# Performance work log

Measured on AMD Instinct MI355X. Metric: run time of the kernel, lower is better.

Reference implementation:

```python
import jax, jax.numpy as jnp
import numpy as np

BLOCK_CONFIGS = [[4, 64, 64], [64, 128, 128], [128, 256, 256], [256, 512]]
KNN_K = 16
PN, PL, PM = 5, 3, 3          # kernel polynomial degrees (N, L, M)
BASIS = PN * PL * PM          # 45 monomial basis functions
NUM_LAYERS = 4
N_POINTS = 32768


def get_reduction_schedule(n_input, n_target, num_layers):
    # geometric point-count reduction from n_input down to n_target
    r = (n_target / n_input) ** (1.0 / num_layers)
    return [max(n_target, int(round(n_input * r ** (i + 1)))) for i in range(num_layers)]


def knn_idx(qpos, spos, k):
    # squared distances via the |q|^2 + |s|^2 - 2 q.s identity (avoids (q,s,3) temp)
    d = jnp.sum(qpos * qpos, 1)[:, None] + jnp.sum(spos * spos, 1)[None, :] - 2.0 * (qpos @ spos.T)
    _, idx = jax.lax.top_k(-d, k)  # (q, k) nearest-neighbor indices
    return idx


def poly_basis(r):
    # monomial basis x^i y^j z^k, i<PN, j<PL, k<PM -> (q, k, BASIS)
    x, y, z = r[..., 0], r[..., 1], r[..., 2]
    px = x[..., None] ** jnp.arange(PN)
    py = y[..., None] ** jnp.arange(PL)
    pz = z[..., None] ** jnp.arange(PM)
    phi = px[..., :, None, None] * py[..., None, :, None] * pz[..., None, None, :]
    return phi.reshape(r.shape[:-1] + (BASIS,))


def dcconv(qpos, spos, sfeat, k, W, b, use_pca=True):
    # KNN gather -> normalized relative coords -> (PCA align) -> polynomial kernel conv
    idx = knn_idx(qpos, spos, k)
    r = spos[idx] - qpos[:, None, :]                         # (q, k, 3)
    scale = jnp.max(jnp.sqrt(jnp.sum(r * r, -1)), axis=-1, keepdims=True)
    r = r / (scale[..., None] + 1e-8)
    if use_pca:
        cov = jnp.einsum('qki,qkj->qij', r, r) / k           # (q, 3, 3)
        _, vecs = jnp.linalg.eigh(cov)
        vecs = jax.lax.stop_gradient(vecs)                   # PCA frame treated as constant
        r = jnp.einsum('qki,qij->qkj', r, vecs)
    phi = poly_basis(r)                                       # (q, k, B)
    nf = sfeat[idx]                                           # (q, k, Cin)
    t = jnp.einsum('qkb,qkc->qbc', phi, nf) / k               # neighbor reduce (mean)
    return jnp.einsum('qbc,bco->qo', t, W) + b


def _forward(position_matrix, channel_matrix, ws, bs, ps, head_w, head_b):
    sched = get_reduction_schedule(position_matrix.shape[0], 1, NUM_LAYERS)
    pos, feat = position_matrix, channel_matrix
    li = 0
    for bi, cfg in enumerate(BLOCK_CONFIGS):
        n_sel = sched[bi]
        qpos = pos[:n_sel]                                    # selector: first n_sel centers
        res = feat[:n_sel] @ ps[bi]                           # residual projection
        x, src_pos = feat, pos
        for _ in range(len(cfg) - 1):
            k = min(KNN_K, src_pos.shape[0])
            x = jax.nn.relu(dcconv(qpos, src_pos, x, k, ws[li], bs[li]))
            li += 1
            src_pos = qpos                                    # subsequent layers: self-conv on reduced set
        feat = jax.nn.relu(x + res)
        pos = qpos
    if feat.shape[0] > 1:
        feat = feat.mean(0, keepdims=True)
    return (feat @ head_w + head_b)[0]                        # (out_channels,) = (1,)


def setup_inputs():
    key = jax.random.key(0)
    ks = jax.random.split(key, 32)
    inp = {}
    inp['position_matrix'] = jax.random.normal(ks[0], (N_POINTS, 3), dtype=jnp.float32)
    inp['channel_matrix'] = jax.random.normal(ks[1], (N_POINTS, 4), dtype=jnp.float32)
    i, li = 2, 1
    for cfg in BLOCK_CONFIGS:
        for cin, cout in zip(cfg[:-1], cfg[1:]):
            inp[f'w{li}'] = jax.random.normal(ks[i], (BASIS, cin, cout), dtype=jnp.float32) * 0.05
            inp[f'b{li}'] = jnp.zeros((cout,), dtype=jnp.float32)
            i += 1
            li += 1
    for bi, cfg in enumerate(BLOCK_CONFIGS):
        inp[f'p{bi + 1}'] = jax.random.normal(ks[i], (cfg[0], cfg[-1]), dtype=jnp.float32) * 0.05
        i += 1
    inp['head_w'] = jax.random.normal(ks[i], (BLOCK_CONFIGS[-1][-1], 1), dtype=jnp.float32) * 0.05
    inp['head_b'] = jnp.zeros((1,), dtype=jnp.float32)
    return inp


def reference(position_matrix, channel_matrix, w1, b1, w2, b2, w3, b3, w4, b4, w5, b5, w6, b6, w7, b7,
              p1, p2, p3, p4, head_w, head_b):
    ws = [w1, w2, w3, w4, w5, w6, w7]
    bs = [b1, b2, b3, b4, b5, b6, b7]
    ps = [p1, p2, p3, p4]
    return _forward(position_matrix, channel_matrix, ws, bs, ps, head_w, head_b)
```

## Files before the change

kernel.cpp:

```cpp
#include <hip/hip_runtime.h>
#include <math.h>

#pragma clang fp contract(off)

__device__ __forceinline__ float f_sign(float a, float b) {
    return (b >= 0.0f) ? fabsf(a) : -fabsf(a);
}

__device__ float slapy2(float x, float y) {
    float xa = fabsf(x), ya = fabsf(y);
    float w = fmaxf(xa, ya), z = fminf(xa, ya);
    if (z == 0.0f) return w;
    float t = z / w;
    return w * sqrtf(1.0f + t * t);
}

__device__ void slartg(float f, float g, float &cs, float &sn, float &r) {
    if (g == 0.0f) { cs = 1.0f; sn = 0.0f; r = f; }
    else if (f == 0.0f) { cs = 0.0f; sn = f_sign(1.0f, g); r = fabsf(g); }
    else {
        float d = sqrtf(f * f + g * g);
        float p = 1.0f / d;
        cs = fabsf(f) * p;
        sn = g * f_sign(p, f);
        r = f_sign(d, f);
    }
}

__device__ void slaev2(float a, float b, float c,
                       float &rt1, float &rt2, float &cs1, float &sn1) {
    float sm = a + c, df = a - c, adf = fabsf(df), tb = b + b, ab = fabsf(tb);
    float acmx, acmn;
    if (fabsf(a) > fabsf(c)) { acmx = a; acmn = c; } else { acmx = c; acmn = a; }
    float rt;
    if (adf > ab) { float t = ab / adf; rt = adf * sqrtf(1.0f + t * t); }
    else if (adf < ab) { float t = adf / ab; rt = ab * sqrtf(1.0f + t * t); }
    else rt = ab * sqrtf(2.0f);
    int sgn1;
    if (sm < 0.0f) { rt1 = 0.5f * (sm - rt); sgn1 = -1; rt2 = (acmx / rt1) * acmn - (b / rt1) * b; }
    else if (sm > 0.0f) { rt1 = 0.5f * (sm + rt); sgn1 = 1; rt2 = (acmx / rt1) * acmn - (b / rt1) * b; }
    else { rt1 = 0.5f * rt; rt2 = -0.5f * rt; sgn1 = 1; }
    float cs; int sgn2;
    if (df >= 0.0f) { cs = df + rt; sgn2 = 1; } else { cs = df - rt; sgn2 = -1; }
    float acs = fabsf(cs);
    if (acs > ab) { float ct = -tb / cs; sn1 = 1.0f / sqrtf(1.0f + ct * ct); cs1 = ct * sn1; }
    else {
        if (ab == 0.0f) { cs1 = 1.0f; sn1 = 0.0f; }
        else { float tn = -cs / tb; cs1 = 1.0f / sqrtf(1.0f + tn * tn); sn1 = tn * cs1; }
    }
    if (sgn1 == sgn2) { float tn = cs1; cs1 = -sn1; sn1 = tn; }
}

__device__ void ssteqr3(float *d, float *e, float z[3][3]) {
    const int n = 3;
    const float eps = 5.9604644775390625e-08f;
    const float eps2 = eps * eps;
    const float safmin = 1.1754943508222875e-38f;
    for (int i = 0; i < 3; ++i)
        for (int j = 0; j < 3; ++j)
            z[i][j] = (i == j) ? 1.0f : 0.0f;
    const int nmaxit = n * 30;
    int jtot = 0;
    int l1 = 1;
    int l, m, lend;
    float p, g, r, c, s, f, b, rt1, rt2;
    float wc[2], wsn[2];

L10:
    if (l1 > n) goto L160;
    if (l1 > 1) e[l1 - 2] = 0.0f;
    if (l1 <= n - 1) {
        for (m = l1; m <= n - 1; ++m) {
            float tst = fabsf(e[m - 1]);
            if (tst == 0.0f) goto L30;
            if (tst <= (sqrtf(fabsf(d[m - 1])) * sqrtf(fabsf(d[m]))) * eps) {
                e[m - 1] = 0.0f;
                goto L30;
            }
        }
    }
    m = n;
L30:
    l = l1;
    lend = m;
    l1 = m + 1;
    if (lend == l) goto L10;
    {
        float anorm = 0.0f;
        for (int i = l; i <= lend; ++i) anorm = fmaxf(anorm, fabsf(d[i - 1]));
        for (int i = l; i <= lend - 1; ++i) anorm = fmaxf(anorm, fabsf(e[i - 1]));
        if (anorm == 0.0f) goto L10;
    }
    if (fabsf(d[lend - 1]) < fabsf(d[l - 1])) { int t = lend; lend = l; l = t; }

    if (lend > l) {
L40:
        if (l != lend) {
            bool found = false;
            for (m = l; m <= lend - 1; ++m) {
                float tst = e[m - 1] * e[m - 1];
                if (tst <= (eps2 * fabsf(d[m - 1])) * fabsf(d[m]) + safmin) { found = true; break; }
            }
            if (!found) m = lend;
        } else m = lend;
        if (m < lend) e[m - 1] = 0.0f;
        p = d[l - 1];
        if (m == l) goto L80;
        if (m == l + 1) {
            slaev2(d[l - 1], e[l - 1], d[l], rt1, rt2, c, s);
            for (int i = 0; i < n; ++i) {
                float tmp = z[i][l];
                z[i][l]     = c * tmp - s * z[i][l - 1];
                z[i][l - 1] = s * tmp + c * z[i][l - 1];
            }
            d[l - 1] = rt1; d[l] = rt2; e[l - 1] = 0.0f;
            l += 2;
            if (l <= lend) goto L40;
            goto L140;
        }
        if (jtot == nmaxit) goto L140;
        ++jtot;
        g = (d[l] - p) / (2.0f * e[l - 1]);
        r = slapy2(g, 1.0f);
        g = (d[m - 1] - p) + e[l - 1] / (g + f_sign(r, g));
        s = 1.0f; c = 1.0f; p = 0.0f;
        for (int i = m - 1; i >= l; --i) {
            f = s * e[i - 1];
            b = c * e[i - 1];
            slartg(g, f, c, s, r);
            if (i != m - 1) e[i] = r;
            g = d[i] - p;
            r = (d[i - 1] - g) * s + (2.0f * c) * b;
            p = s * r;
            d[i] = g + p;
            g = c * r - b;
            wc[i - 1] = c;
            wsn[i - 1] = -s;
        }
        for (int jj = m - 1; jj >= l; --jj) {
            float ct = wc[jj - 1], st = wsn[jj - 1];
            for (int i = 0; i < n; ++i) {
                float tmp = z[i][jj];
                z[i][jj]     = ct * tmp - st * z[i][jj - 1];
                z[i][jj - 1] = st * tmp + ct * z[i][jj - 1];
            }
        }
        d[l - 1] -= p;
        e[l - 1] = g;
        goto L40;
L80:
        d[l - 1] = p;
        ++l;
        if (l <= lend) goto L40;
        goto L140;
    } else {
L90:
        if (l != lend) {
            bool found = false;
            for (m = l; m >= lend + 1; --m) {
                float tst = e[m - 2] * e[m - 2];
                if (tst <= (eps2 * fabsf(d[m - 1])) * fabsf(d[m - 2]) + safmin) { found = true; break; }
            }
            if (!found) m = lend;
        } else m = lend;
        if (m > lend) e[m - 2] = 0.0f;
        p = d[l - 1];
        if (m == l) goto L130;
        if (m == l - 1) {
            slaev2(d[l - 2], e[l - 2], d[l - 1], rt1, rt2, c, s);
            for (int i = 0; i < n; ++i) {
                float tmp = z[i][l - 1];
                z[i][l - 1] = c * tmp - s * z[i][l - 2];
                z[i][l - 2] = s * tmp + c * z[i][l - 2];
            }
            d[l - 2] = rt1; d[l - 1] = rt2; e[l - 2] = 0.0f;
            l -= 2;
            if (l >= lend) goto L90;
            goto L140;
        }
        if (jtot == nmaxit) goto L140;
        ++jtot;
        g = (d[l - 2] - p) / (2.0f * e[l - 2]);
        r = slapy2(g, 1.0f);
        g = (d[m - 1] - p) + e[l - 2] / (g + f_sign(r, g));
        s = 1.0f; c = 1.0f; p = 0.0f;
        for (int i = m; i <= l - 1; ++i) {
            f = s * e[i - 1];
            b = c * e[i - 1];
            slartg(g, f, c, s, r);
            if (i != m) e[i - 2] = r;
            g = d[i - 1] - p;
            r = (d[i] - g) * s + (2.0f * c) * b;
            p = s * r;
            d[i - 1] = g + p;
            g = c * r - b;
            wc[i - 1] = c;
            wsn[i - 1] = s;
        }
        for (int jj = m; jj <= l - 1; ++jj) {
            float ct = wc[jj - 1], st = wsn[jj - 1];
            for (int i = 0; i < n; ++i) {
                float tmp = z[i][jj];
                z[i][jj]     = ct * tmp - st * z[i][jj - 1];
                z[i][jj - 1] = st * tmp + ct * z[i][jj - 1];
            }
        }
        d[l - 1] -= p;
        e[l - 2] = g;
        goto L90;
L130:
        d[l - 1] = p;
        --l;
        if (l >= lend) goto L90;
        goto L140;
    }
L140:
    if (jtot < nmaxit) goto L10;
L160:
    for (int ii = 2; ii <= n; ++ii) {
        int i = ii - 1, kk = i;
        float pp = d[i - 1];
        for (int j = ii; j <= n; ++j)
            if (d[j - 1] < pp) { kk = j; pp = d[j - 1]; }
        if (kk != i) {
            d[kk - 1] = d[i - 1];
            d[i - 1] = pp;
            for (int row = 0; row < n; ++row) {
                float t2 = z[row][i - 1];
                z[row][i - 1] = z[row][kk - 1];
                z[row][kk - 1] = t2;
            }
        }
    }
}

__device__ void ssyevd3(float a11, float a21, float a31,
                        float a22, float a32, float a33, float V[3][3]) {
    float tau1, v2, e1;
    float alpha = a21;
    float xnorm = fabsf(a31);
    if (xnorm == 0.0f) {
        tau1 = 0.0f; v2 = 0.0f; e1 = a21;
    } else {
        float beta = -f_sign(slapy2(alpha, xnorm), alpha);
        tau1 = (beta - alpha) / beta;
        float t = 1.0f / (alpha - beta);
        v2 = a31 * t;
        e1 = beta;
        float w1 = tau1 * a22;
        float w2 = tau1 * a32;
        float temp2 = a32 * v2;
        w1 = w1 + tau1 * temp2;
        float temp1 = tau1 * v2;
        w2 = w2 + temp1 * a33;
        float dot = w1;
        dot = dot + w2 * v2;
        float alpha2 = (-0.5f * tau1) * dot;
        w1 = w1 + alpha2;
        w2 = w2 + alpha2 * v2;
        a22 = (a22 - w1) - w1;
        a32 = (a32 - v2 * w1) - w2;
        a33 = (a33 - v2 * w2) - w2 * v2;
    }
    float d[3] = { a11, a22, a33 };
    float e[2] = { e1, a32 };
    float z[3][3];
    ssteqr3(d, e, z);
    for (int j = 0; j < 3; ++j) {
        float wj = z[1][j];
        wj = wj + z[2][j] * v2;
        float temp = (-tau1) * wj;
        V[0][j] = z[0][j];
        V[1][j] = z[1][j] + temp;
        V[2][j] = z[2][j] + v2 * temp;
    }
}

__device__ void geom_body(const float *__restrict__ posf, const int *__restrict__ ord,
                          int q, int k, float *__restrict__ rrot) {
    float qx = posf[3 * q], qy = posf[3 * q + 1], qz = posf[3 * q + 2];
    float rx[16], ry[16], rz[16], nrm[16];
    for (int j = 0; j < k; ++j) {
        int s = ord[j];
        rx[j] = posf[3 * s] - qx;
        ry[j] = posf[3 * s + 1] - qy;
        rz[j] = posf[3 * s + 2] - qz;
        float t = rx[j] * rx[j];
        t = t + ry[j] * ry[j];
        t = t + rz[j] * rz[j];
        nrm[j] = sqrtf(t);
    }
    float scale = nrm[0];
    for (int j = 1; j < k; ++j) scale = fmaxf(scale, nrm[j]);
    float sc = scale + 1e-8f;
    for (int j = 0; j < k; ++j) {
        rx[j] = rx[j] / sc;
        ry[j] = ry[j] / sc;
        rz[j] = rz[j] / sc;
    }
    float c00 = 0.f, c01 = 0.f, c02 = 0.f, c11 = 0.f, c12 = 0.f, c22 = 0.f;
    for (int j = 0; j < k; ++j) {
        c00 = c00 + rx[j] * rx[j];
        c01 = c01 + rx[j] * ry[j];
        c02 = c02 + rx[j] * rz[j];
        c11 = c11 + ry[j] * ry[j];
        c12 = c12 + ry[j] * rz[j];
        c22 = c22 + rz[j] * rz[j];
    }
    float fk = (float)k;
    c00 = c00 / fk; c01 = c01 / fk; c02 = c02 / fk;
    c11 = c11 / fk; c12 = c12 / fk; c22 = c22 / fk;
    float V[3][3];
    ssyevd3(c00, c01, c02, c11, c12, c22, V);
    for (int j = 0; j < k; ++j) {
        for (int col = 0; col < 3; ++col) {
            float a = rx[j] * V[0][col];
            a = a + ry[j] * V[1][col];
            a = a + rz[j] * V[2][col];
            rrot[q * 48 + j * 3 + col] = a;
        }
    }
}

__global__ __launch_bounds__(256) void geom_kernel(
    const float *__restrict__ posf, const int *__restrict__ idx,
    int Q, int k, float *__restrict__ rrot) {
    int q = blockIdx.x * 256 + threadIdx.x;
    if (q >= Q) return;
    geom_body(posf, idx + (size_t)q * k, q, k, rrot);
}


__global__ void prep_kernel(const float *__restrict__ posf, float4 *__restrict__ pos4) {
    int i = blockIdx.x * 256 + threadIdx.x;
    if (i >= 32768) return;
    float x = posf[3 * i], y = posf[3 * i + 1], z = posf[3 * i + 2];
    float t = x * x;
    t = t + y * y;
    t = t + z * z;
    pos4[i] = make_float4(x, y, z, t);
}

__device__ __forceinline__ void insert16(float d, int jbase, int lane,
                                         float &ld, int &li, float &kth) {
    unsigned long long mask = __ballot(d < kth);
    while (mask) {
        int src = __ffsll(mask) - 1;
        mask &= mask - 1;
        float dv = __int_as_float(__builtin_amdgcn_readlane(__float_as_int(d), src));
        int jv = jbase + src;
        if (dv < kth) {
            unsigned long long lm = __ballot((lane < 16) && (ld <= dv));
            int p2 = __popcll(lm);
            float sd = __int_as_float(__builtin_amdgcn_update_dpp(
                0, __float_as_int(ld), 0x111, 0xf, 0xf, true));
            int si = __builtin_amdgcn_update_dpp(0, li, 0x111, 0xf, 0xf, true);
            if (lane < 16) {
                if (lane == p2) { ld = dv; li = jv; }
                else if (lane > p2) { ld = sd; li = si; }
            }
            kth = __int_as_float(__builtin_amdgcn_readlane(__float_as_int(ld), 15));
        }
    }
}

__device__ __forceinline__ void sort64_init(float d, int jbase, int lane,
                                            float &ld, int &li, float &kth) {
    float v = d;
    int vi = jbase + lane;
#pragma unroll
    for (int k2 = 2; k2 <= 64; k2 <<= 1) {
#pragma unroll
        for (int j2 = k2 >> 1; j2 > 0; j2 >>= 1) {
            float ov = __shfl_xor(v, j2);
            int oi = __shfl_xor(vi, j2);
            bool oless = (ov < v) || (ov == v && oi < vi);
            bool dir = ((lane & k2) == 0);
            bool keepmin = (((lane & j2) == 0) == dir);
            bool take = keepmin ? oless : !oless;
            if (take) { v = ov; vi = oi; }
        }
    }
    if (lane < 16) { ld = v; li = vi; }
    kth = __int_as_float(__builtin_amdgcn_readlane(__float_as_int(v), 15));
}

__device__ __forceinline__ void scan_range(
    const float4 *__restrict__ pos4, float4 qp, int start, int end, int lane,
    float &ld, int &li, float &kth) {
    const float FINF = 3.0e38f;
    int base = start;
    float4 c0, c1, c2, c3;
    bool have = (base + 256 <= end);
    bool first = true;
    if (have) {
        c0 = pos4[base + lane];
        c1 = pos4[base + 64 + lane];
        c2 = pos4[base + 128 + lane];
        c3 = pos4[base + 192 + lane];
    }
    while (have) {
        int nbase = base + 1024;
        bool nhave = (nbase + 256 <= end);
        float4 n0 = c0, n1 = c1, n2 = c2, n3 = c3;
        if (nhave) {
            n0 = pos4[nbase + lane];
            n1 = pos4[nbase + 64 + lane];
            n2 = pos4[nbase + 128 + lane];
            n3 = pos4[nbase + 192 + lane];
        }
        float m0 = fmaf(qp.x, c0.x, 0.0f);
        m0 = fmaf(qp.y, c0.y, m0);
        m0 = fmaf(qp.z, c0.z, m0);
        float d0 = (qp.w + c0.w) - 2.0f * m0;
        float m1 = fmaf(qp.x, c1.x, 0.0f);
        m1 = fmaf(qp.y, c1.y, m1);
        m1 = fmaf(qp.z, c1.z, m1);
        float d1 = (qp.w + c1.w) - 2.0f * m1;
        float m2 = fmaf(qp.x, c2.x, 0.0f);
        m2 = fmaf(qp.y, c2.y, m2);
        m2 = fmaf(qp.z, c2.z, m2);
        float d2 = (qp.w + c2.w) - 2.0f * m2;
        float m3 = fmaf(qp.x, c3.x, 0.0f);
        m3 = fmaf(qp.y, c3.y, m3);
        m3 = fmaf(qp.z, c3.z, m3);
        float d3 = (qp.w + c3.w) - 2.0f * m3;
        float dmin = fminf(fminf(d0, d1), fminf(d2, d3));
        if (first || __ballot(dmin < kth)) {
            if (first) {
                sort64_init(d0, base, lane, ld, li, kth);
                first = false;
            } else {
                insert16(d0, base, lane, ld, li, kth);
            }
            insert16(d1, base + 64, lane, ld, li, kth);
            insert16(d2, base + 128, lane, ld, li, kth);
            insert16(d3, base + 192, lane, ld, li, kth);
        }
        c0 = n0; c1 = n1; c2 = n2; c3 = n3;
        base = nbase;
        have = nhave;
    }
    if (base < end) {
#pragma unroll
        for (int k2 = 0; k2 < 4; ++k2) {
            int j = base + k2 * 64 + lane;
            float dd = FINF;
            if (j < end) {
                float4 p = pos4[j];
                float m = fmaf(qp.x, p.x, 0.0f);
                m = fmaf(qp.y, p.y, m);
                m = fmaf(qp.z, p.z, m);
                dd = (qp.w + p.w) - 2.0f * m;
            }
            insert16(dd, base + k2 * 64, lane, ld, li, kth);
        }
    }
}

__device__ __forceinline__ void merge4x16(const float *md, const int *mi,
                                          int lane, float &v2, int &vi2) {
    int l16 = lane & 15;
    int srcA = (lane >> 5) * 32 + ((lane & 16) ? (16 + (15 - l16)) : l16);
    float v = md[srcA];
    int vi = mi[srcA];
    for (int off = 16; off > 0; off >>= 1) {
        float ov = __shfl_xor(v, off);
        int oi = __shfl_xor(vi, off);
        bool oless = (ov < v) || (ov == v && oi < vi);
        bool take = (lane & off) ? (!oless) : oless;
        if (take) { v = ov; vi = oi; }
    }
    int src2 = (lane < 16) ? lane : (63 - lane);
    v2 = __shfl(v, src2);
    vi2 = __shfl(vi, src2);
    for (int off = 16; off > 0; off >>= 1) {
        float ov = __shfl_xor(v2, off);
        int oi = __shfl_xor(vi2, off);
        bool oless = (ov < v2) || (ov == v2 && oi < vi2);
        bool take = (lane & off) ? (!oless) : oless;
        if (take) { v2 = ov; vi2 = oi; }
    }
}

__global__ __launch_bounds__(256) void knng16_kernel(
    const float4 *__restrict__ pos4, int S, int *__restrict__ idx_out) {
    __shared__ float md[64];
    __shared__ int mi[64];
    int q = blockIdx.x;
    int tid = threadIdx.x;
    int lane = tid & 63;
    int w = tid >> 6;
    float4 qp = pos4[q];
    const float FINF = 3.0e38f;
    float ld = FINF;
    int li = 0x7fffffff;
    float kth = FINF;
    scan_range(pos4, qp, w * 256, S, lane, ld, li, kth);
    if (lane < 16) { md[w * 16 + lane] = ld; mi[w * 16 + lane] = li; }
    __syncthreads();
    if (w == 0) {
        float v2; int vi2;
        merge4x16(md, mi, lane, v2, vi2);
        if (lane < 16) idx_out[q * 16 + lane] = vi2;
    }
}

__global__ __launch_bounds__(64) void knngs_kernel(
    const float4 *__restrict__ pos4, int S, int k, int *__restrict__ idx_out) {
    int q = blockIdx.x;
    int lane = threadIdx.x;
    float4 qp = pos4[q];
    const float FINF = 3.0e38f;
    float dist = FINF;
    if (lane < S) {
        float4 p = pos4[lane];
        float m = fmaf(qp.x, p.x, 0.0f);
        m = fmaf(qp.y, p.y, m);
        m = fmaf(qp.z, p.z, m);
        dist = (qp.w + p.w) - 2.0f * m;
    }
    bool used = false;
    for (int r = 0; r < k; ++r) {
        float v = used ? FINF : dist;
        int vid = (used || lane >= S) ? 0x7fffffff : lane;
        for (int off = 32; off > 0; off >>= 1) {
            float ov = __shfl_down(v, off);
            int oid = __shfl_down(vid, off);
            if (ov < v || (ov == v && oid < vid)) { v = ov; vid = oid; }
        }
        vid = __shfl(vid, 0);
        if (lane == 0) idx_out[q * k + r] = vid;
        if (lane == vid) used = true;
    }
}

__device__ __forceinline__ void compute_phi(const float *rrot, int q, int tid,
                                            double phi[45]) {
    double x = (double)rrot[q * 48 + tid * 3 + 0];
    double y = (double)rrot[q * 48 + tid * 3 + 1];
    double z = (double)rrot[q * 48 + tid * 3 + 2];
    double px[5], py[3], pz[3];
    px[0] = 1.0; px[1] = x; px[2] = x * x; px[3] = px[2] * x; px[4] = px[3] * x;
    py[0] = 1.0; py[1] = y; py[2] = y * y;
    pz[0] = 1.0; pz[1] = z; pz[2] = z * z;
#pragma unroll
    for (int n2 = 0; n2 < 5; ++n2)
#pragma unroll
        for (int l2 = 0; l2 < 3; ++l2)
#pragma unroll
            for (int m2 = 0; m2 < 3; ++m2)
                phi[n2 * 9 + l2 * 3 + m2] = (px[n2] * py[l2]) * pz[m2];
}

__global__ __launch_bounds__(256) void feat_kernel(
    const float *__restrict__ rrot, const int *__restrict__ idx, int k,
    const double *__restrict__ fin64, const float *__restrict__ fin32, int C,
    const float *__restrict__ W, const float *__restrict__ bias, int O,
    double *__restrict__ fout) {
    __shared__ double phi_sh[16][45];
    __shared__ int idx_sh[16];
    __shared__ double red_sh[256];
    extern __shared__ double dyn[];
    double *nf = dyn;
    double *t = dyn + 16 * C;
    int q = blockIdx.x;
    int tid = threadIdx.x;
    int OT = O < 256 ? O : 256;
    int nseg = 256 / OT;
    int o = tid % OT;
    int seg = tid / OT;
    int cseg = C / nseg;
    int c0 = seg * cseg, c1 = c0 + cseg;
    if (tid < k) {
        idx_sh[tid] = idx[q * k + tid];
        double phi[45];
        compute_phi(rrot, q, tid, phi);
#pragma unroll
        for (int b2 = 0; b2 < 45; ++b2) phi_sh[tid][b2] = phi[b2];
    }
    __syncthreads();
    for (int e2 = tid; e2 < k * C; e2 += 256) {
        int j = e2 / C, cc = e2 - j * C;
        size_t src = (size_t)idx_sh[j] * C + cc;
        nf[j * C + cc] = fin32 ? (double)fin32[src] : fin64[src];
    }
    __syncthreads();
    double accp = 0.0;
    for (int ch = 0; ch < 45; ch += 9) {
        for (int e2 = tid; e2 < 9 * C; e2 += 256) {
            int b2 = e2 / C, cc = e2 - b2 * C;
            double a2 = 0.0;
            for (int j = 0; j < k; ++j) a2 = fma(phi_sh[j][ch + b2], nf[j * C + cc], a2);
            t[e2] = a2 / (double)k;
        }
        __syncthreads();
        double a0 = 0.0, a1 = 0.0;
        for (int b2 = 0; b2 < 9; ++b2) {
            const float *wp = W + (size_t)(ch + b2) * C * O + o;
            const double *tp = t + b2 * C;
            int cc = c0;
            for (; cc + 2 <= c1; cc += 2) {
                a0 = fma(tp[cc],     (double)wp[(size_t)cc * O], a0);
                a1 = fma(tp[cc + 1], (double)wp[(size_t)(cc + 1) * O], a1);
            }
            for (; cc < c1; ++cc) a0 = fma(tp[cc], (double)wp[(size_t)cc * O], a0);
        }
        accp += a0 + a1;
        __syncthreads();
    }
    red_sh[tid] = accp;
    __syncthreads();
    if (tid < OT) {
        double v = 0.0;
        for (int s2 = 0; s2 < nseg; ++s2) v += red_sh[tid + s2 * OT];
        v += (double)bias[tid];
        fout[(size_t)q * O + tid] = v > 0.0 ? v : 0.0;
    }
}

__global__ __launch_bounds__(256) void feat64_kernel(
    const float *__restrict__ rrot, const int *__restrict__ idx,
    const double *__restrict__ fin, const float *__restrict__ W,
    const float *__restrict__ bias, int Q, double *__restrict__ fout) {
    __shared__ double phi_sh[2][16][45];
    __shared__ int idx_sh[2][16];
    __shared__ double nf[2][16][64];
    __shared__ double t[2][9][64];
    __shared__ double red[16][64];
    int q0 = blockIdx.x * 2;
    int nq = (Q - q0) < 2 ? (Q - q0) : 2;
    int tid = threadIdx.x;
    int tx = tid & 15;
    int seg = tid >> 4;
    int o0 = tx * 4;
    int cbase = seg * 4;
    if (tid < 32) {
        int qi = tid >> 4, j = tid & 15;
        int qq = q0 + (qi < nq ? qi : 0);
        idx_sh[qi][j] = idx[qq * 16 + j];
        double phi[45];
        compute_phi(rrot, qq, j, phi);
#pragma unroll
        for (int b2 = 0; b2 < 45; ++b2) phi_sh[qi][j][b2] = phi[b2];
    }
    __syncthreads();
    for (int e2 = tid; e2 < 2 * 16 * 64; e2 += 256) {
        int qi = e2 >> 10, j = (e2 >> 6) & 15, cc = e2 & 63;
        nf[qi][j][cc] = fin[(size_t)idx_sh[qi][j] * 64 + cc];
    }
    __syncthreads();
    double acc[2][4] = {{0.0, 0.0, 0.0, 0.0}, {0.0, 0.0, 0.0, 0.0}};
    for (int ch = 0; ch < 45; ch += 9) {
        for (int e2 = tid; e2 < 2 * 9 * 64; e2 += 256) {
            int qi = e2 / 576, rem = e2 - qi * 576;
            int b2 = rem >> 6, cc = rem & 63;
            double a2 = 0.0;
#pragma unroll
            for (int j = 0; j < 16; ++j) a2 = fma(phi_sh[qi][j][ch + b2], nf[qi][j][cc], a2);
            t[qi][b2][cc] = a2 * 0.0625;
        }
        __syncthreads();
#pragma unroll
        for (int b2 = 0; b2 < 9; ++b2) {
            const float *wrow = W + ((size_t)(ch + b2) * 64 + cbase) * 64 + o0;
#pragma unroll
            for (int i = 0; i < 4; ++i) {
                float4 wv = *(const float4 *)(wrow + (size_t)i * 64);
                double w0 = (double)wv.x, w1 = (double)wv.y;
                double w2 = (double)wv.z, w3 = (double)wv.w;
                double tv0 = t[0][b2][cbase + i];
                double tv1 = t[1][b2][cbase + i];
                acc[0][0] = fma(tv0, w0, acc[0][0]);
                acc[0][1] = fma(tv0, w1, acc[0][1]);
                acc[0][2] = fma(tv0, w2, acc[0][2]);
                acc[0][3] = fma(tv0, w3, acc[0][3]);
                acc[1][0] = fma(tv1, w0, acc[1][0]);
                acc[1][1] = fma(tv1, w1, acc[1][1]);
                acc[1][2] = fma(tv1, w2, acc[1][2]);
                acc[1][3] = fma(tv1, w3, acc[1][3]);
            }
        }
        __syncthreads();
    }
    for (int qi = 0; qi < nq; ++qi) {
        red[seg][o0 + 0] = acc[qi][0];
        red[seg][o0 + 1] = acc[qi][1];
        red[seg][o0 + 2] = acc[qi][2];
        red[seg][o0 + 3] = acc[qi][3];
        __syncthreads();
        if (tid < 64) {
            double v = 0.0;
#pragma unroll
            for (int s2 = 0; s2 < 16; ++s2) v += red[s2][tid];
            v += (double)bias[tid];
            fout[(size_t)(q0 + qi) * 64 + tid] = v > 0.0 ? v : 0.0;
        }
        __syncthreads();
    }
}

__global__ __launch_bounds__(256) void t_kernel(
    const float *__restrict__ rrot, const int *__restrict__ idx, int k,
    const double *__restrict__ fin, int C, int q0, double *__restrict__ tbuf,
    double *__restrict__ fout, int O) {
    __shared__ double phi_sh[16][45];
    __shared__ int idx_sh[16];
    extern __shared__ double nf[];
    int q = q0 + blockIdx.x;
    int bch = blockIdx.y * 9;
    int tid = threadIdx.x;
    if (blockIdx.y == 0) {
        for (int i = tid; i < O; i += 256) fout[(size_t)q * O + i] = 0.0;
    }
    if (tid < k) {
        idx_sh[tid] = idx[q * k + tid];
        double phi[45];
        compute_phi(rrot, q, tid, phi);
#pragma unroll
        for (int b2 = 0; b2 < 45; ++b2) phi_sh[tid][b2] = phi[b2];
    }
    __syncthreads();
    for (int e2 = tid; e2 < k * C; e2 += 256) {
        int j = e2 / C, cc = e2 - j * C;
        nf[j * C + cc] = fin[(size_t)idx_sh[j] * C + cc];
    }
    __syncthreads();
    int K = 45 * C;
    for (int e2 = tid; e2 < 9 * C; e2 += 256) {
        int b2 = bch + e2 / C, cc = e2 % C;
        double a2 = 0.0;
        for (int j = 0; j < k; ++j) a2 = fma(phi_sh[j][b2], nf[j * C + cc], a2);
        tbuf[(size_t)blockIdx.x * K + b2 * C + cc] = a2 / (double)k;
    }
}

__global__ __launch_bounds__(256) void gemm_kernel(
    const double *__restrict__ tbuf, const float *__restrict__ W,
    int K, int O, int q0, int q1, int kchunk, double *__restrict__ acc) {
    int OT = O < 256 ? O : 256;
    int qpb = 256 / OT;
    int tid = threadIdx.x;
    int o = blockIdx.x * OT + (tid % OT);
    int q = q0 + blockIdx.y * qpb + tid / OT;
    if (q >= q1) return;
    int k0 = blockIdx.z * kchunk;
    if (k0 >= K) return;
    int kend = min(k0 + kchunk, K);
    const double *tp = tbuf + (size_t)(q - q0) * K;
    const float *wp = W + (size_t)k0 * O + o;
    double a0 = 0.0, a1 = 0.0, a2 = 0.0, a3 = 0.0;
    double a4 = 0.0, a5 = 0.0, a6 = 0.0, a7 = 0.0;
    int kk = k0;
    for (; kk + 8 <= kend; kk += 8) {
        double2 t01 = *(const double2 *)(tp + kk);
        double2 t23 = *(const double2 *)(tp + kk + 2);
        double2 t45 = *(const double2 *)(tp + kk + 4);
        double2 t67 = *(const double2 *)(tp + kk + 6);
        float w0 = wp[0];
        float w1 = wp[(size_t)O];
        float w2 = wp[2 * (size_t)O];
        float w3 = wp[3 * (size_t)O];
        float w4 = wp[4 * (size_t)O];
        float w5 = wp[5 * (size_t)O];
        float w6 = wp[6 * (size_t)O];
        float w7 = wp[7 * (size_t)O];
        a0 = fma(t01.x, (double)w0, a0);
        a1 = fma(t01.y, (double)w1, a1);
        a2 = fma(t23.x, (double)w2, a2);
        a3 = fma(t23.y, (double)w3, a3);
        a4 = fma(t45.x, (double)w4, a4);
        a5 = fma(t45.y, (double)w5, a5);
        a6 = fma(t67.x, (double)w6, a6);
        a7 = fma(t67.y, (double)w7, a7);
        wp += 8 * (size_t)O;
    }
    for (; kk < kend; ++kk) {
        a0 = fma(tp[kk], (double)wp[0], a0);
        wp += (size_t)O;
    }
    double s = ((a0 + a1) + (a2 + a3)) + ((a4 + a5) + (a6 + a7));
    atomicAdd(&acc[(size_t)q * O + o], s);
}

__global__ void finalize_kernel(const float *__restrict__ bias,
                                int Q, int O, double *__restrict__ fout) {
    int i = blockIdx.x * 256 + threadIdx.x;
    if (i >= Q * O) return;
    int o = i % O;
    double v = fout[i] + (double)bias[o];
    fout[i] = v > 0.0 ? v : 0.0;
}

__global__ void resid0_kernel(const float *__restrict__ chanf, const float *__restrict__ p,
                              const double *__restrict__ x, double *__restrict__ fout) {
    int i = blockIdx.x * 256 + threadIdx.x;
    if (i >= 2435 * 64) return;
    int q = i >> 6, o = i & 63;
    const float *f = chanf + 4 * q;
    float c = fmaf(f[0], p[o], 0.0f);
    c = fmaf(f[1], p[64 + o], c);
    c = fmaf(f[2], p[128 + o], c);
    c = fmaf(f[3], p[192 + o], c);
    double v = x[i] + (double)c;
    fout[i] = v > 0.0 ? v : 0.0;
}

__global__ void resid64f_kernel(const float *__restrict__ bias,
                                const double *__restrict__ acc,
                                const double *__restrict__ fin, int Cin,
                                const float *__restrict__ p,
                                int Q, int Cout, double *__restrict__ fout) {
    int i = blockIdx.x * blockDim.x + threadIdx.x;
    if (i >= Q * Cout) return;
    int q = i / Cout, o = i - q * Cout;
    double v = acc[i] + (double)bias[o];
    double x = v > 0.0 ? v : 0.0;
    double a = 0.0;
    for (int c = 0; c < Cin; ++c) a = fma(fin[q * Cin + c], (double)p[c * Cout + o], a);
    double r = x + a;
    fout[i] = r > 0.0 ? r : 0.0;
}

__global__ void head_kernel(const double *__restrict__ feat, const float *__restrict__ hw,
                            const float *__restrict__ hb, float *__restrict__ out) {
    if (threadIdx.x == 0 && blockIdx.x == 0) {
        double acc = 0.0;
        for (int c = 0; c < 512; ++c) acc = fma(feat[c], (double)hw[c], acc);
        out[0] = (float)(acc + (double)hb[0]);
    }
}


extern "C" void kernel_launch(void *const *d_in, const int *in_sizes, int n_in,
                              void *d_out, int out_size, void *d_ws, size_t ws_size,
                              hipStream_t stream) {
    (void)in_sizes; (void)n_in; (void)out_size;

    const float *posf = (const float *)d_in[0];
    const float *chanf = (const float *)d_in[1];
    const float *W[8], *B[8];
    for (int li = 1; li <= 7; ++li) {
        W[li] = (const float *)d_in[2 + 2 * (li - 1)];
        B[li] = (const float *)d_in[3 + 2 * (li - 1)];
    }
    const float *P[5];
    for (int bi = 1; bi <= 4; ++bi) P[bi] = (const float *)d_in[15 + bi];
    const float *hw = (const float *)d_in[20];
    const float *hb = (const float *)d_in[21];

    char *wsb = (char *)d_ws;
    double *B1   = (double *)(wsb + 0);
    double *B2   = (double *)(wsb + 1246720);
    double *B3   = (double *)(wsb + 2493440);
    float *rrot  = (float *)(wsb + 3740160);
    int *idx     = (int *)(wsb + 4207680);
    float4 *pos4 = (float4 *)(wsb + 4363520);
    double *tbuf = (double *)(wsb + 4887808);
    if (ws_size < 9082112) return;

    prep_kernel<<<128, 256, 0, stream>>>(posf, pos4);

    auto knng = [&](int Q, int S, int k) {
        if (S <= 64)
            knngs_kernel<<<Q, 64, 0, stream>>>(pos4, S, k, idx);
        else
            knng16_kernel<<<Q, 256, 0, stream>>>(pos4, S, idx);
        geom_kernel<<<(Q + 255) / 256, 256, 0, stream>>>(posf, idx, Q, k, rrot);
    };

    auto conv = [&](int Q, int S, int k, const double *fin64, const float *fin32, int C,
                    const float *w, const float *bias, int O, double *fout) {
        knng(Q, S, k);
        size_t dyn = (size_t)(16 + 9) * C * sizeof(double);
        feat_kernel<<<Q, 256, dyn, stream>>>(rrot, idx, k, fin64, fin32, C, w, bias, O, fout);
    };

    auto conv64 = [&](int Q, int S, const double *fin, const float *w,
                      const float *bias, double *fout) {
        knng(Q, S, 16);
        feat64_kernel<<<(Q + 1) / 2, 256, 0, stream>>>(rrot, idx, fin, w, bias, Q, fout);
    };

    auto conv2 = [&](int Q, int S, int k, const double *fin, int C,
                     const float *w, const float *bias, int O, double *fout,
                     int ksplit, bool do_finalize, bool skip_knn) {
        if (!skip_knn) knng(Q, S, k);
        int K = 45 * C;
        int qc = 4194304 / (K * 8);
        if (qc > Q) qc = Q;
        int OT = O < 256 ? O : 256;
        int qpb = 256 / OT;
        int kchunk = (((K + ksplit - 1) / ksplit) + 7) & ~7;
        for (int q0 = 0; q0 < Q; q0 += qc) {
            int qn = min(qc, Q - q0);
            dim3 gt(qn, 5);
            t_kernel<<<gt, 256, (size_t)16 * C * sizeof(double), stream>>>(
                rrot, idx, k, fin, C, q0, tbuf, fout, O);
            dim3 g(O / OT, (qn + qpb - 1) / qpb, ksplit);
            gemm_kernel<<<g, 256, 0, stream>>>(tbuf, w, K, O, q0, q0 + qn, kchunk, fout);
        }
        if (do_finalize)
            finalize_kernel<<<(Q * O + 255) / 256, 256, 0, stream>>>(bias, Q, O, fout);
    };

    conv(2435, 32768, 16, nullptr, chanf, 4, W[1], B[1], 64, B1);
    conv64(2435, 2435, B1, W[2], B[2], B2);
    resid0_kernel<<<(2435 * 64 + 255) / 256, 256, 0, stream>>>(chanf, P[1], B2, B3);
    conv2(181, 2435, 16, B3, 64, W[3], B[3], 128, B1, 24, true, true);
    conv2(181, 181, 16, B1, 128, W[4], B[4], 128, B2, 24, false, false);
    resid64f_kernel<<<(181 * 128 + 255) / 256, 256, 0, stream>>>(
        B[4], B2, B3, 64, P[2], 181, 128, B1);
    conv2(13, 181, 16, B1, 128, W[5], B[5], 256, B2, 96, true, true);
    conv2(13, 13, 13, B2, 256, W[6], B[6], 256, B3, 96, false, false);
    resid64f_kernel<<<(13 * 256 + 255) / 256, 256, 0, stream>>>(
        B[6], B3, B1, 128, P[3], 13, 256, B2);
    conv2(1, 13, 13, B2, 256, W[7], B[7], 512, B1, 256, false, true);
    resid64f_kernel<<<(1 * 512 + 255) / 256, 256, 0, stream>>>(
        B[7], B1, B2, 256, P[4], 1, 512, B3);

    head_kernel<<<1, 64, 0, stream>>>(B3, hw, hb, (float *)d_out);
}
```

Baseline: 790.8 us.

## Fuse geometry into KNN, bias-ReLU into gather, resid into head; raise ksplit

```diff
diff --git a/kernel.cpp b/kernel.cpp
--- a/kernel.cpp
+++ b/kernel.cpp
@@ -483,10 +483,13 @@
     }
 }
 
+template <int DOGEOM>
 __global__ __launch_bounds__(256) void knng16_kernel(
-    const float4 *__restrict__ pos4, int S, int *__restrict__ idx_out) {
+    const float4 *__restrict__ pos4, const float *__restrict__ posf,
+    int S, int *__restrict__ idx_out, float *__restrict__ rrot) {
     __shared__ float md[64];
     __shared__ int mi[64];
+    __shared__ int ord[16];
     int q = blockIdx.x;
     int tid = threadIdx.x;
     int lane = tid & 63;
@@ -502,12 +505,18 @@
     if (w == 0) {
         float v2; int vi2;
         merge4x16(md, mi, lane, v2, vi2);
-        if (lane < 16) idx_out[q * 16 + lane] = vi2;
+        if (lane < 16) {
+            idx_out[q * 16 + lane] = vi2;
+            if (DOGEOM) ord[lane] = vi2;
+        }
+        if (DOGEOM && lane == 0) geom_body(posf, ord, q, 16, rrot);
     }
 }
 
 __global__ __launch_bounds__(64) void knngs_kernel(
-    const float4 *__restrict__ pos4, int S, int k, int *__restrict__ idx_out) {
+    const float4 *__restrict__ pos4, const float *__restrict__ posf,
+    int S, int k, int *__restrict__ idx_out, float *__restrict__ rrot) {
+    __shared__ int ord[16];
     int q = blockIdx.x;
     int lane = threadIdx.x;
     float4 qp = pos4[q];
@@ -530,9 +539,10 @@
             if (ov < v || (ov == v && oid < vid)) { v = ov; vid = oid; }
         }
         vid = __shfl(vid, 0);
-        if (lane == 0) idx_out[q * k + r] = vid;
+        if (lane == 0) { idx_out[q * k + r] = vid; ord[r] = vid; }
         if (lane == vid) used = true;
     }
+    if (lane == 0) geom_body(posf, ord, q, k, rrot);
 }
 
 __device__ __forceinline__ void compute_phi(const float *rrot, int q, int tid,
@@ -702,8 +712,8 @@
 
 __global__ __launch_bounds__(256) void t_kernel(
     const float *__restrict__ rrot, const int *__restrict__ idx, int k,
-    const double *__restrict__ fin, int C, int q0, double *__restrict__ tbuf,
-    double *__restrict__ fout, int O) {
+    const double *__restrict__ fin, const float *__restrict__ fbias, int C,
+    int q0, double *__restrict__ tbuf, double *__restrict__ fout, int O) {
     __shared__ double phi_sh[16][45];
     __shared__ int idx_sh[16];
     extern __shared__ double nf[];
@@ -723,7 +733,12 @@
     __syncthreads();
     for (int e2 = tid; e2 < k * C; e2 += 256) {
         int j = e2 / C, cc = e2 - j * C;
-        nf[j * C + cc] = fin[(size_t)idx_sh[j] * C + cc];
+        double v = fin[(size_t)idx_sh[j] * C + cc];
+        if (fbias) {
+            v = v + (double)fbias[cc];
+            v = v > 0.0 ? v : 0.0;
+        }
+        nf[j * C + cc] = v;
     }
     __syncthreads();
     int K = 45 * C;
@@ -783,15 +798,6 @@
     atomicAdd(&acc[(size_t)q * O + o], s);
 }
 
-__global__ void finalize_kernel(const float *__restrict__ bias,
-                                int Q, int O, double *__restrict__ fout) {
-    int i = blockIdx.x * 256 + threadIdx.x;
-    if (i >= Q * O) return;
-    int o = i % O;
-    double v = fout[i] + (double)bias[o];
-    fout[i] = v > 0.0 ? v : 0.0;
-}
-
 __global__ void resid0_kernel(const float *__restrict__ chanf, const float *__restrict__ p,
                               const double *__restrict__ x, double *__restrict__ fout) {
     int i = blockIdx.x * 256 + threadIdx.x;
@@ -822,12 +828,32 @@
     fout[i] = r > 0.0 ? r : 0.0;
 }
 
-__global__ void head_kernel(const double *__restrict__ feat, const float *__restrict__ hw,
-                            const float *__restrict__ hb, float *__restrict__ out) {
-    if (threadIdx.x == 0 && blockIdx.x == 0) {
-        double acc = 0.0;
-        for (int c = 0; c < 512; ++c) acc = fma(feat[c], (double)hw[c], acc);
-        out[0] = (float)(acc + (double)hb[0]);
+__global__ __launch_bounds__(512) void resid_head_kernel(
+    const float *__restrict__ bias, const double *__restrict__ acc,
+    const double *__restrict__ fin, int Cin, const float *__restrict__ p,
+    const float *__restrict__ hw, const float *__restrict__ hb,
+    float *__restrict__ out) {
+    __shared__ double rv[512];
+    __shared__ double red[64];
+    int i = threadIdx.x;
+    double v = acc[i] + (double)bias[i];
+    double x = v > 0.0 ? v : 0.0;
+    double a = 0.0;
+    for (int c = 0; c < Cin; ++c) a = fma(fin[c], (double)p[c * 512 + i], a);
+    double r = x + a;
+    r = r > 0.0 ? r : 0.0;
+    rv[i] = r * (double)hw[i];
+    __syncthreads();
+    if (i < 64) {
+        double s = 0.0;
+        for (int j = 0; j < 8; ++j) s += rv[i * 8 + j];
+        red[i] = s;
+    }
+    __syncthreads();
+    if (i == 0) {
+        double s = 0.0;
+        for (int j = 0; j < 64; ++j) s += red[j];
+        out[0] = (float)(s + (double)hb[0]);
     }
 }
 
@@ -862,11 +888,14 @@
     prep_kernel<<<128, 256, 0, stream>>>(posf, pos4);
 
     auto knng = [&](int Q, int S, int k) {
-        if (S <= 64)
-            knngs_kernel<<<Q, 64, 0, stream>>>(pos4, S, k, idx);
-        else
-            knng16_kernel<<<Q, 256, 0, stream>>>(pos4, S, idx);
-        geom_kernel<<<(Q + 255) / 256, 256, 0, stream>>>(posf, idx, Q, k, rrot);
+        if (S <= 64) {
+            knngs_kernel<<<Q, 64, 0, stream>>>(pos4, posf, S, k, idx, rrot);
+        } else if (Q >= 512) {
+            knng16_kernel<0><<<Q, 256, 0, stream>>>(pos4, posf, S, idx, rrot);
+            geom_kernel<<<(Q + 255) / 256, 256, 0, stream>>>(posf, idx, Q, k, rrot);
+        } else {
+            knng16_kernel<1><<<Q, 256, 0, stream>>>(pos4, posf, S, idx, rrot);
+        }
     };
 
     auto conv = [&](int Q, int S, int k, const double *fin64, const float *fin32, int C,
@@ -882,9 +911,9 @@
         feat64_kernel<<<(Q + 1) / 2, 256, 0, stream>>>(rrot, idx, fin, w, bias, Q, fout);
     };
 
-    auto conv2 = [&](int Q, int S, int k, const double *fin, int C,
-                     const float *w, const float *bias, int O, double *fout,
-                     int ksplit, bool do_finalize, bool skip_knn) {
+    auto conv2 = [&](int Q, int S, int k, const double *fin, const float *fbias,
+                     int C, const float *w, int O, double *fout,
+                     int ksplit, bool skip_knn) {
         if (!skip_knn) knng(Q, S, k);
         int K = 45 * C;
         int qc = 4194304 / (K * 8);
@@ -896,28 +925,24 @@
             int qn = min(qc, Q - q0);
             dim3 gt(qn, 5);
             t_kernel<<<gt, 256, (size_t)16 * C * sizeof(double), stream>>>(
-                rrot, idx, k, fin, C, q0, tbuf, fout, O);
+                rrot, idx, k, fin, fbias, C, q0, tbuf, fout, O);
             dim3 g(O / OT, (qn + qpb - 1) / qpb, ksplit);
             gemm_kernel<<<g, 256, 0, stream>>>(tbuf, w, K, O, q0, q0 + qn, kchunk, fout);
         }
-        if (do_finalize)
-            finalize_kernel<<<(Q * O + 255) / 256, 256, 0, stream>>>(bias, Q, O, fout);
     };
 
     conv(2435, 32768, 16, nullptr, chanf, 4, W[1], B[1], 64, B1);
     conv64(2435, 2435, B1, W[2], B[2], B2);
     resid0_kernel<<<(2435 * 64 + 255) / 256, 256, 0, stream>>>(chanf, P[1], B2, B3);
-    conv2(181, 2435, 16, B3, 64, W[3], B[3], 128, B1, 24, true, true);
-    conv2(181, 181, 16, B1, 128, W[4], B[4], 128, B2, 24, false, false);
+    conv2(181, 2435, 16, B3, nullptr, 64, W[3], 128, B1, 48, true);
+    conv2(181, 181, 16, B1, B[3], 128, W[4], 128, B2, 48, false);
     resid64f_kernel<<<(181 * 128 + 255) / 256, 256, 0, stream>>>(
         B[4], B2, B3, 64, P[2], 181, 128, B1);
-    conv2(13, 181, 16, B1, 128, W[5], B[5], 256, B2, 96, true, true);
-    conv2(13, 13, 13, B2, 256, W[6], B[6], 256, B3, 96, false, false);
+    conv2(13, 181, 16, B1, nullptr, 128, W[5], 256, B2, 160, true);
+    conv2(13, 13, 13, B2, B[5], 256, W[6], 256, B3, 160, false);
     resid64f_kernel<<<(13 * 256 + 255) / 256, 256, 0, stream>>>(
         B[6], B3, B1, 128, P[3], 13, 256, B2);
-    conv2(1, 13, 13, B2, 256, W[7], B[7], 512, B1, 256, false, true);
-    resid64f_kernel<<<(1 * 512 + 255) / 256, 256, 0, stream>>>(
-        B[7], B1, B2, 256, P[4], 1, 512, B3);
-
-    head_kernel<<<1, 64, 0, stream>>>(B3, hw, hb, (float *)d_out);
-}
+    conv2(1, 13, 13, B2, nullptr, 256, W[7], 512, B1, 320, true);
+    resid_head_kernel<<<1, 512, 0, stream>>>(B[7], B1, B2, 256, P[4], hw, hb,
+                                             (float *)d_out);
+}
```

New measurement: 796.5 us. About the same (+0.7%).
